# Performance work log

Measured on AMD Instinct MI355X. Metric: run time of the kernel, lower is better.

## Reference

```python
import jax, jax.numpy as jnp
import numpy as np

NEG_SLOPE = 0.2

def _glorot(key, shape):
    fan_in, fan_out = shape[0], shape[1]
    lim = (6.0 / (fan_in + fan_out)) ** 0.5
    return jax.random.uniform(key, shape, jnp.float32, -lim, lim)

def setup_inputs() -> dict:
    key = jax.random.key(0)
    N, E = 50000, 1000000
    node_dim, edge_dim, hidden = 64, 16, 32
    H1 = 4
    ks = jax.random.split(key, 20)
    x = jax.random.normal(ks[0], (N, node_dim), jnp.float32)
    edge_index = jax.random.randint(ks[1], (2, E), 0, N, jnp.int64)
    edge_attr = jax.random.normal(ks[2], (E, edge_dim), jnp.float32)
    d = dict(x=x, edge_index=edge_index, edge_attr=edge_attr)
    # gat1: GATv2Conv(node_dim -> hidden, heads=4, edge_dim)
    d['W1l'] = _glorot(ks[3], (node_dim, H1 * hidden)); d['b1l'] = jnp.zeros((H1 * hidden,), jnp.float32)
    d['W1r'] = _glorot(ks[4], (node_dim, H1 * hidden)); d['b1r'] = jnp.zeros((H1 * hidden,), jnp.float32)
    d['W1e'] = _glorot(ks[5], (edge_dim, H1 * hidden))
    d['att1'] = _glorot(ks[6], (H1, hidden))
    d['bias1'] = jnp.zeros((H1 * hidden,), jnp.float32)
    # gat2: GATv2Conv(4*hidden -> hidden, heads=1, edge_dim)
    d['W2l'] = _glorot(ks[7], (H1 * hidden, hidden)); d['b2l'] = jnp.zeros((hidden,), jnp.float32)
    d['W2r'] = _glorot(ks[8], (H1 * hidden, hidden)); d['b2r'] = jnp.zeros((hidden,), jnp.float32)
    d['W2e'] = _glorot(ks[9], (edge_dim, hidden))
    d['att2'] = _glorot(ks[10], (1, hidden))
    d['bias2'] = jnp.zeros((hidden,), jnp.float32)
    # edge classifier: Linear(2*hidden+edge_dim -> hidden), ReLU, Linear(hidden -> 1)
    ein = 2 * hidden + edge_dim
    d['Wc1'] = _glorot(ks[11], (ein, hidden)); d['bc1'] = jnp.zeros((hidden,), jnp.float32)
    d['Wc2'] = _glorot(ks[12], (hidden, 1)); d['bc2'] = jnp.zeros((1,), jnp.float32)
    return d

def _gatv2(x, src, dst, eattr, Wl, bl, Wr, br, We, att, bias, H, C):
    # src/dst already include self loops; eattr matches.
    N = x.shape[0]
    xl = (x @ Wl + bl).reshape(N, H, C)   # source transform
    xr = (x @ Wr + br).reshape(N, H, C)   # target transform
    ea = (eattr @ We).reshape(-1, H, C)
    m = jax.nn.leaky_relu(xl[src] + xr[dst] + ea, NEG_SLOPE)   # [E,H,C]
    alpha = jnp.einsum('ehc,hc->eh', m, att)                   # [E,H]
    amax = jax.ops.segment_max(alpha, dst, num_segments=N)
    ealpha = jnp.exp(alpha - amax[dst])
    denom = jax.ops.segment_sum(ealpha, dst, num_segments=N)
    alpha = ealpha / denom[dst]
    out = jax.ops.segment_sum(xl[src] * alpha[..., None], dst, num_segments=N)
    return out.reshape(N, H * C) + bias

def reference(x, edge_index, edge_attr, W1l, b1l, W1r, b1r, W1e, att1, bias1,
              W2l, b2l, W2r, b2r, W2e, att2, bias2, Wc1, bc1, Wc2, bc2):
    N = x.shape[0]
    src, dst = edge_index[0], edge_index[1]
    # add self loops with edge_attr fill_value='mean' (per-target mean of incoming edge attrs)
    loop_attr = jax.ops.segment_sum(edge_attr, dst, num_segments=N)
    deg = jax.ops.segment_sum(jnp.ones((dst.shape[0],), edge_attr.dtype), dst, num_segments=N)
    loop_attr = loop_attr / jnp.maximum(deg, 1.0)[:, None]
    ar = jnp.arange(N, dtype=src.dtype)
    src2 = jnp.concatenate([src, ar]); dst2 = jnp.concatenate([dst, ar])
    eattr2 = jnp.concatenate([edge_attr, loop_attr], axis=0)
    h = _gatv2(x, src2, dst2, eattr2, W1l, b1l, W1r, b1r, W1e, att1, bias1, 4, 32)
    h = jax.nn.elu(h)
    h = _gatv2(h, src2, dst2, eattr2, W2l, b2l, W2r, b2r, W2e, att2, bias2, 1, 32)
    h = jax.nn.elu(h)
    edge_emb = jnp.concatenate([h[src], h[dst]], axis=1)         # [E, 2*hidden]
    feats = jnp.concatenate([edge_emb, edge_attr], axis=1)       # [E, 2*hidden+edge_dim]
    hid = jax.nn.relu(feats @ Wc1 + bc1)
    logits = (hid @ Wc2 + bc2).squeeze(-1)                        # [E]
    return logits
```

## Files before the change

kernel.cpp:

```cpp
#include <hip/hip_runtime.h>

namespace {

constexpr int NN  = 50000;
constexpr int EE  = 1000000;
constexpr int EE2 = EE + NN;
constexpr int ND  = 64;
constexpr int F1  = 128;
constexpr int F2  = 32;
constexpr float NEG = 0.2f;

typedef unsigned short ushort_t;
typedef _Float16 half_t;
typedef _Float16 half2_t __attribute__((ext_vector_type(2)));

__device__ __forceinline__ unsigned short f2h(float f) {
  union { half_t h; unsigned short u; } c; c.h = (half_t)f; return c.u;
}
__device__ __forceinline__ float h2f(unsigned short v) {
  union { unsigned short u; half_t h; } c; c.u = v; return (float)c.h;
}
__device__ __forceinline__ half2_t u2h2(unsigned u) {
  union { unsigned u; half2_t h; } c; c.u = u; return c.h;
}
__device__ __forceinline__ unsigned pack2(float x, float y) {
  return (unsigned)f2h(x) | ((unsigned)f2h(y) << 16);
}
__device__ __forceinline__ half2_t mkh2(float x, float y) {
  half2_t r; r.x = (half_t)x; r.y = (half_t)y; return r;
}

#if __has_builtin(__builtin_amdgcn_fdot2)
#define FDOT2(a, b, c) __builtin_amdgcn_fdot2((a), (b), (c), false)
#else
#define FDOT2(a, b, c) ((float)(a).x * (float)(b).x + (float)(a).y * (float)(b).y + (c))
#endif

__global__ __launch_bounds__(256) void k_deg(const int* __restrict__ ei,
                                             int* __restrict__ deg) {
  int e = blockIdx.x * 256 + threadIdx.x;
  if (e < EE) atomicAdd(&deg[ei[EE + e]], 1);
}

__global__ __launch_bounds__(1024) void k_scan(const int* __restrict__ deg,
                                               int* __restrict__ rowstart) {
  __shared__ int sh[1024];
  int t = threadIdx.x;
  int base = t * 49;
  int end = base + 49; if (end > NN) end = NN;
  int s = 0;
  for (int i = base; i < end; ++i) s += deg[i] + 1;
  sh[t] = s;
  __syncthreads();
  for (int off = 1; off < 1024; off <<= 1) {
    int v = (t >= off) ? sh[t - off] : 0;
    __syncthreads();
    sh[t] += v;
    __syncthreads();
  }
  int run = (t == 0) ? 0 : sh[t - 1];
  for (int i = base; i < end; ++i) { rowstart[i] = run; run += deg[i] + 1; }
  if (t == 1023) rowstart[NN] = sh[1023];
}

__global__ __launch_bounds__(256) void k_fill(const int* __restrict__ ei,
                                              const float* __restrict__ edge_attr,
                                              const int* __restrict__ rowstart,
                                              int* __restrict__ cursor,
                                              int2* __restrict__ esd,
                                              ushort_t* __restrict__ eperm,
                                              int* __restrict__ loopos) {
  int i = blockIdx.x * 256 + threadIdx.x;
  if (i >= EE2) return;
  int sn, d;
  if (i < EE) { sn = ei[i]; d = ei[EE + i]; }
  else        { sn = i - EE; d = sn; }
  int pos = rowstart[d] + atomicAdd(&cursor[d], 1);
  esd[pos] = make_int2(sn, d);
  if (i < EE) {
    const float4* s4 = (const float4*)(edge_attr + (size_t)i * 16);
    float4 a = s4[0], b = s4[1], c = s4[2], e = s4[3];
    uint4 lo, hi;
    lo.x = pack2(a.x, a.y); lo.y = pack2(a.z, a.w);
    lo.z = pack2(b.x, b.y); lo.w = pack2(b.z, b.w);
    hi.x = pack2(c.x, c.y); hi.y = pack2(c.z, c.w);
    hi.z = pack2(e.x, e.y); hi.w = pack2(e.z, e.w);
    uint4* t4 = (uint4*)(eperm + (size_t)pos * 16);
    t4[0] = lo; t4[1] = hi;
  } else {
    loopos[d] = pos;
  }
}

__global__ __launch_bounds__(256) void k_loopattr(const int* __restrict__ rowstart,
                                                  const int* __restrict__ loopos,
                                                  ushort_t* __restrict__ eperm) {
  int tid = blockIdx.x * 256 + threadIdx.x;
  if (tid >= NN * 16) return;
  int n = tid >> 4, k = tid & 15;
  int s = rowstart[n], t = rowstart[n + 1];
  int lp = loopos[n];
  float acc = 0.f;
  for (int i = s; i < t; ++i) {
    if (i != lp) acc += h2f(eperm[(size_t)i * 16 + k]);
  }
  float dg = (float)(t - s - 1);
  eperm[(size_t)lp * 16 + k] = f2h(acc / fmaxf(dg, 1.f));
}

__global__ __launch_bounds__(256) void k_xprep(const float* __restrict__ x,
                                               unsigned* __restrict__ xh) {
  int tid = blockIdx.x * 256 + threadIdx.x;
  if (tid >= NN * 32) return;
  float2 v = ((const float2*)x)[tid];
  xh[tid] = pack2(v.x, v.y);
}

__global__ __launch_bounds__(256) void k_wprep(const float* __restrict__ W1l,
                                               const float* __restrict__ W1r,
                                               const float* __restrict__ W2l,
                                               const float* __restrict__ W2r,
                                               unsigned* __restrict__ W1lp,
                                               unsigned* __restrict__ W1rp,
                                               unsigned* __restrict__ W2lp,
                                               unsigned* __restrict__ W2rp) {
  int tid = blockIdx.x * 256 + threadIdx.x;
  if (tid < 32 * 128) {
    int kp = tid >> 7, j = tid & 127;
    W1lp[tid] = pack2(W1l[(2 * kp) * F1 + j], W1l[(2 * kp + 1) * F1 + j]);
    W1rp[tid] = pack2(W1r[(2 * kp) * F1 + j], W1r[(2 * kp + 1) * F1 + j]);
  }
  if (tid < 64 * 32) {
    int kp = tid >> 5, c = tid & 31;
    W2lp[tid] = pack2(W2l[(2 * kp) * F2 + c], W2l[(2 * kp + 1) * F2 + c]);
    W2rp[tid] = pack2(W2r[(2 * kp) * F2 + c], W2r[(2 * kp + 1) * F2 + c]);
  }
}

__global__ __launch_bounds__(256) void k_xform1(const unsigned* __restrict__ xh,
                                                const unsigned* __restrict__ W1lp,
                                                const unsigned* __restrict__ W1rp,
                                                const float* __restrict__ b1l,
                                                const float* __restrict__ b1r,
                                                ushort_t* __restrict__ xlh,
                                                ushort_t* __restrict__ xrh) {
  int tid = blockIdx.x * 256 + threadIdx.x;
  if (tid >= NN * 32) return;
  int n = tid >> 5, g = tid & 31;
  float4 bl = *(const float4*)(b1l + 4 * g);
  float4 br = *(const float4*)(b1r + 4 * g);
  float al0 = bl.x, al1 = bl.y, al2 = bl.z, al3 = bl.w;
  float ar0 = br.x, ar1 = br.y, ar2 = br.z, ar3 = br.w;
  const uint4* xp = (const uint4*)(xh + (size_t)n * 32);
  const uint4* wl = (const uint4*)W1lp;
  const uint4* wr = (const uint4*)W1rp;
#pragma unroll
  for (int kq = 0; kq < 8; ++kq) {
    uint4 xq = xp[kq];
    unsigned xs[4] = {xq.x, xq.y, xq.z, xq.w};
#pragma unroll
    for (int i = 0; i < 4; ++i) {
      int kp = 4 * kq + i;
      uint4 a = wl[kp * 32 + g];
      uint4 b = wr[kp * 32 + g];
      half2_t xv = u2h2(xs[i]);
      al0 = FDOT2(xv, u2h2(a.x), al0);
      al1 = FDOT2(xv, u2h2(a.y), al1);
      al2 = FDOT2(xv, u2h2(a.z), al2);
      al3 = FDOT2(xv, u2h2(a.w), al3);
      ar0 = FDOT2(xv, u2h2(b.x), ar0);
      ar1 = FDOT2(xv, u2h2(b.y), ar1);
      ar2 = FDOT2(xv, u2h2(b.z), ar2);
      ar3 = FDOT2(xv, u2h2(b.w), ar3);
    }
  }
  uint2 ol, orr;
  ol.x = pack2(al0, al1); ol.y = pack2(al2, al3);
  orr.x = pack2(ar0, ar1); orr.y = pack2(ar2, ar3);
  *(uint2*)(xlh + (size_t)n * F1 + 4 * g) = ol;
  *(uint2*)(xrh + (size_t)n * F1 + 4 * g) = orr;
}

__global__ __launch_bounds__(256, 4) void k_alpha1(const ushort_t* __restrict__ eperm,
                                                   const int2* __restrict__ esd,
                                                   const ushort_t* __restrict__ xlh,
                                                   const ushort_t* __restrict__ xrh,
                                                   const float* __restrict__ W1e,
                                                   const float* __restrict__ att1,
                                                   float* __restrict__ alpha1) {
  int lane = threadIdx.x & 63;
  int h = lane >> 4, q = lane & 15, j = h * 32 + 2 * q;
  half2_t w0p[8], w1p[8];
#pragma unroll
  for (int k = 0; k < 8; ++k) {
    w0p[k] = mkh2(W1e[(2 * k) * F1 + j],     W1e[(2 * k + 1) * F1 + j]);
    w1p[k] = mkh2(W1e[(2 * k) * F1 + j + 1], W1e[(2 * k + 1) * F1 + j + 1]);
  }
  float a0 = att1[j], a1 = att1[j + 1];
  int wid = (blockIdx.x * 256 + threadIdx.x) >> 6;
  int nw  = (gridDim.x * 256) >> 6;
  if (wid >= EE2) return;
  const int last = EE2 - 1;

  int2 sd1 = esd[min(wid + nw, last)];
  int2 sd0 = esd[wid];
  const uint4* ep0 = (const uint4*)(eperm + (size_t)wid * 16);
  uint4 ca = ep0[0], cb = ep0[1];
  unsigned ul = *(const unsigned*)(xlh + (size_t)sd0.x * F1 + j);
  unsigned ur = *(const unsigned*)(xrh + (size_t)sd0.y * F1 + j);

  for (int pos = wid; pos <= last; pos += nw) {
    int2 sd2 = esd[min(pos + 2 * nw, last)];
    const uint4* epn = (const uint4*)(eperm + (size_t)min(pos + nw, last) * 16);
    uint4 na = epn[0], nb = epn[1];
    unsigned uln = *(const unsigned*)(xlh + (size_t)sd1.x * F1 + j);
    unsigned urn = *(const unsigned*)(xrh + (size_t)sd1.y * F1 + j);
    half2_t e2[8];
    e2[0] = u2h2(ca.x); e2[1] = u2h2(ca.y); e2[2] = u2h2(ca.z); e2[3] = u2h2(ca.w);
    e2[4] = u2h2(cb.x); e2[5] = u2h2(cb.y); e2[6] = u2h2(cb.z); e2[7] = u2h2(cb.w);
    float ea0 = 0.f, ea1 = 0.f;
#pragma unroll
    for (int k = 0; k < 8; ++k) {
      ea0 = FDOT2(e2[k], w0p[k], ea0);
      ea1 = FDOT2(e2[k], w1p[k], ea1);
    }
    half2_t ul2 = u2h2(ul), ur2 = u2h2(ur);
    float m0 = (float)ul2.x + (float)ur2.x + ea0;
    float m1 = (float)ul2.y + (float)ur2.y + ea1;
    m0 = fmaxf(m0, NEG * m0);
    m1 = fmaxf(m1, NEG * m1);
    float p = a0 * m0 + a1 * m1;
#pragma unroll
    for (int m = 8; m >= 1; m >>= 1) p += __shfl_xor(p, m);
    if (q == 0) alpha1[(size_t)pos * 4 + h] = p;
    sd1 = sd2; ca = na; cb = nb; ul = uln; ur = urn;
  }
}

__global__ __launch_bounds__(256) void k_gatB1(const int2* __restrict__ esd,
                                               const int* __restrict__ rowstart,
                                               const float* __restrict__ alpha1,
                                               const ushort_t* __restrict__ xlh,
                                               const float* __restrict__ bias1,
                                               unsigned* __restrict__ h1h) {
  int n = (blockIdx.x * 256 + threadIdx.x) >> 6;
  if (n >= NN) return;
  int lane = threadIdx.x & 63;
  int h = lane >> 4;
  int s = rowstart[n], t = rowstart[n + 1];
  const int* srcp = (const int*)esd;
  float d = 0.f, acc0 = 0.f, acc1 = 0.f;
  for (int i = s; i < t; i += 4) {
    int i1 = min(i + 1, t - 1), i2 = min(i + 2, t - 1), i3 = min(i + 3, t - 1);
    int s0 = srcp[2 * i], s1 = srcp[2 * i1], s2 = srcp[2 * i2], s3 = srcp[2 * i3];
    float A0 = alpha1[(size_t)i * 4 + h];
    float A1 = alpha1[(size_t)i1 * 4 + h];
    float A2 = alpha1[(size_t)i2 * 4 + h];
    float A3 = alpha1[(size_t)i3 * 4 + h];
    unsigned g0 = *(const unsigned*)(xlh + (size_t)s0 * F1 + 2 * lane);
    unsigned g1 = *(const unsigned*)(xlh + (size_t)s1 * F1 + 2 * lane);
    unsigned g2 = *(const unsigned*)(xlh + (size_t)s2 * F1 + 2 * lane);
    unsigned g3 = *(const unsigned*)(xlh + (size_t)s3 * F1 + 2 * lane);
    float W0 = __expf(A0);
    float W1 = (i + 1 < t) ? __expf(A1) : 0.f;
    float W2 = (i + 2 < t) ? __expf(A2) : 0.f;
    float W3 = (i + 3 < t) ? __expf(A3) : 0.f;
    d += W0 + W1 + W2 + W3;
    half2_t h0 = u2h2(g0), h1v = u2h2(g1), h2v = u2h2(g2), h3v = u2h2(g3);
    acc0 += (float)h0.x * W0 + (float)h1v.x * W1 + (float)h2v.x * W2 + (float)h3v.x * W3;
    acc1 += (float)h0.y * W0 + (float)h1v.y * W1 + (float)h2v.y * W2 + (float)h3v.y * W3;
  }
  float2 bs = *(const float2*)(bias1 + 2 * lane);
  float o0 = acc0 / d + bs.x;
  float o1 = acc1 / d + bs.y;
  o0 = o0 > 0.f ? o0 : (__expf(o0) - 1.f);
  o1 = o1 > 0.f ? o1 : (__expf(o1) - 1.f);
  h1h[(size_t)n * 64 + lane] = pack2(o0, o1);
}

__global__ __launch_bounds__(256) void k_xform2(const unsigned* __restrict__ h1h,
                                                const unsigned* __restrict__ W2lp,
                                                const unsigned* __restrict__ W2rp,
                                                const float* __restrict__ b2l,
                                                const float* __restrict__ b2r,
                                                ushort_t* __restrict__ xl2h,
                                                ushort_t* __restrict__ xr2h) {
  int tid = blockIdx.x * 256 + threadIdx.x;
  if (tid >= NN * 8) return;
  int n = tid >> 3, g = tid & 7;
  float4 bl = *(const float4*)(b2l + 4 * g);
  float4 br = *(const float4*)(b2r + 4 * g);
  float al0 = bl.x, al1 = bl.y, al2 = bl.z, al3 = bl.w;
  float ar0 = br.x, ar1 = br.y, ar2 = br.z, ar3 = br.w;
  const uint4* hp = (const uint4*)(h1h + (size_t)n * 64);
  const uint4* wl = (const uint4*)W2lp;
  const uint4* wr = (const uint4*)W2rp;
#pragma unroll 4
  for (int kq = 0; kq < 16; ++kq) {
    uint4 hq = hp[kq];
    unsigned hs[4] = {hq.x, hq.y, hq.z, hq.w};
#pragma unroll
    for (int i = 0; i < 4; ++i) {
      int kp = 4 * kq + i;
      uint4 a = wl[kp * 8 + g];
      uint4 b = wr[kp * 8 + g];
      half2_t hv = u2h2(hs[i]);
      al0 = FDOT2(hv, u2h2(a.x), al0);
      al1 = FDOT2(hv, u2h2(a.y), al1);
      al2 = FDOT2(hv, u2h2(a.z), al2);
      al3 = FDOT2(hv, u2h2(a.w), al3);
      ar0 = FDOT2(hv, u2h2(b.x), ar0);
      ar1 = FDOT2(hv, u2h2(b.y), ar1);
      ar2 = FDOT2(hv, u2h2(b.z), ar2);
      ar3 = FDOT2(hv, u2h2(b.w), ar3);
    }
  }
  uint2 ol, orr;
  ol.x = pack2(al0, al1); ol.y = pack2(al2, al3);
  orr.x = pack2(ar0, ar1); orr.y = pack2(ar2, ar3);
  *(uint2*)(xl2h + (size_t)n * F2 + 4 * g) = ol;
  *(uint2*)(xr2h + (size_t)n * F2 + 4 * g) = orr;
}

__global__ __launch_bounds__(256, 4) void k_alpha2(const ushort_t* __restrict__ eperm,
                                                   const int2* __restrict__ esd,
                                                   const ushort_t* __restrict__ xl2h,
                                                   const ushort_t* __restrict__ xr2h,
                                                   const float* __restrict__ W2e,
                                                   const float* __restrict__ att2,
                                                   float* __restrict__ alpha2) {
  int lane = threadIdx.x & 63;
  int g = lane >> 4, q = lane & 15, j = 2 * q;
  half2_t w0p[8], w1p[8];
#pragma unroll
  for (int k = 0; k < 8; ++k) {
    w0p[k] = mkh2(W2e[(2 * k) * F2 + j],     W2e[(2 * k + 1) * F2 + j]);
    w1p[k] = mkh2(W2e[(2 * k) * F2 + j + 1], W2e[(2 * k + 1) * F2 + j + 1]);
  }
  float a0 = att2[j], a1 = att2[j + 1];
  int wid = (blockIdx.x * 256 + threadIdx.x) >> 6;
  int nw  = (gridDim.x * 256) >> 6;
  const int st = nw * 4;
  const int last = EE2 - 1;
  int base0 = wid * 4;
  if (base0 >= EE2) return;

  int2 sd1 = esd[min(base0 + st + g, last)];
  int2 sd0 = esd[min(base0 + g, last)];
  const uint4* ep0 = (const uint4*)(eperm + (size_t)min(base0 + g, last) * 16);
  uint4 ca = ep0[0], cb = ep0[1];
  unsigned ul = *(const unsigned*)(xl2h + (size_t)sd0.x * F2 + j);
  unsigned ur = *(const unsigned*)(xr2h + (size_t)sd0.y * F2 + j);

  for (int base = base0; base < EE2; base += st) {
    int2 sd2 = esd[min(base + 2 * st + g, last)];
    const uint4* epn = (const uint4*)(eperm + (size_t)min(base + st + g, last) * 16);
    uint4 na = epn[0], nb = epn[1];
    unsigned uln = *(const unsigned*)(xl2h + (size_t)sd1.x * F2 + j);
    unsigned urn = *(const unsigned*)(xr2h + (size_t)sd1.y * F2 + j);
    half2_t e2[8];
    e2[0] = u2h2(ca.x); e2[1] = u2h2(ca.y); e2[2] = u2h2(ca.z); e2[3] = u2h2(ca.w);
    e2[4] = u2h2(cb.x); e2[5] = u2h2(cb.y); e2[6] = u2h2(cb.z); e2[7] = u2h2(cb.w);
    float ea = 0.f, eb = 0.f;
#pragma unroll
    for (int k = 0; k < 8; ++k) {
      ea = FDOT2(e2[k], w0p[k], ea);
      eb = FDOT2(e2[k], w1p[k], eb);
    }
    half2_t ul2 = u2h2(ul), ur2 = u2h2(ur);
    float m0 = (float)ul2.x + (float)ur2.x + ea;
    float m1 = (float)ul2.y + (float)ur2.y + eb;
    m0 = fmaxf(m0, NEG * m0);
    m1 = fmaxf(m1, NEG * m1);
    float p = a0 * m0 + a1 * m1;
#pragma unroll
    for (int m = 8; m >= 1; m >>= 1) p += __shfl_xor(p, m);
    int pos = base + g;
    if (q == 0 && pos < EE2) alpha2[pos] = p;
    sd1 = sd2; ca = na; cb = nb; ul = uln; ur = urn;
  }
}

__global__ __launch_bounds__(256) void k_gatB2(const int2* __restrict__ esd,
                                               const int* __restrict__ rowstart,
                                               const float* __restrict__ alpha2,
                                               const ushort_t* __restrict__ xl2h,
                                               const float* __restrict__ bias2,
                                               float* __restrict__ h2) {
  int n = (blockIdx.x * 256 + threadIdx.x) >> 4;
  if (n >= NN) return;
  int q = threadIdx.x & 15;
  int s = rowstart[n], t = rowstart[n + 1];
  const int* srcp = (const int*)esd;
  float d = 0.f, acc0 = 0.f, acc1 = 0.f;
  for (int i = s; i < t; i += 4) {
    int i1 = min(i + 1, t - 1), i2 = min(i + 2, t - 1), i3 = min(i + 3, t - 1);
    int s0 = srcp[2 * i], s1 = srcp[2 * i1], s2 = srcp[2 * i2], s3 = srcp[2 * i3];
    float A0 = alpha2[i], A1 = alpha2[i1], A2 = alpha2[i2], A3 = alpha2[i3];
    unsigned g0 = *(const unsigned*)(xl2h + (size_t)s0 * F2 + 2 * q);
    unsigned g1 = *(const unsigned*)(xl2h + (size_t)s1 * F2 + 2 * q);
    unsigned g2 = *(const unsigned*)(xl2h + (size_t)s2 * F2 + 2 * q);
    unsigned g3 = *(const unsigned*)(xl2h + (size_t)s3 * F2 + 2 * q);
    float W0 = __expf(A0);
    float W1 = (i + 1 < t) ? __expf(A1) : 0.f;
    float W2 = (i + 2 < t) ? __expf(A2) : 0.f;
    float W3 = (i + 3 < t) ? __expf(A3) : 0.f;
    d += W0 + W1 + W2 + W3;
    half2_t h0 = u2h2(g0), h1v = u2h2(g1), h2v = u2h2(g2), h3v = u2h2(g3);
    acc0 += (float)h0.x * W0 + (float)h1v.x * W1 + (float)h2v.x * W2 + (float)h3v.x * W3;
    acc1 += (float)h0.y * W0 + (float)h1v.y * W1 + (float)h2v.y * W2 + (float)h3v.y * W3;
  }
  float2 bs = *(const float2*)(bias2 + 2 * q);
  float o0 = acc0 / d + bs.x;
  float o1 = acc1 / d + bs.y;
  o0 = o0 > 0.f ? o0 : (__expf(o0) - 1.f);
  o1 = o1 > 0.f ? o1 : (__expf(o1) - 1.f);
  *(float2*)(h2 + (size_t)n * F2 + 2 * q) = make_float2(o0, o1);
}

__global__ __launch_bounds__(256) void k_ucls(const float* __restrict__ h2,
                                              const float* __restrict__ Wc1,
                                              float* __restrict__ us,
                                              float* __restrict__ ud) {
  int tid = blockIdx.x * 256 + threadIdx.x;
  if (tid >= NN * F2) return;
  int n = tid >> 5, c = tid & 31;
  const float* hp = h2 + (size_t)n * F2;
  float a = 0.f, b = 0.f;
#pragma unroll 8
  for (int k = 0; k < 32; ++k) {
    float hv = hp[k];
    a += hv * Wc1[k * F2 + c];
    b += hv * Wc1[(32 + k) * F2 + c];
  }
  us[tid] = a;
  ud[tid] = b;
}

__global__ __launch_bounds__(256, 4) void k_cls(const int* __restrict__ ei,
                                                const float* __restrict__ edge_attr,
                                                const float* __restrict__ us,
                                                const float* __restrict__ ud,
                                                const float* __restrict__ Wc1,
                                                const float* __restrict__ bc1,
                                                const float* __restrict__ Wc2,
                                                const float* __restrict__ bc2,
                                                float* __restrict__ out) {
  int lane = threadIdx.x & 63;
  int g = lane >> 4, q = lane & 15, j = 2 * q;
  float wk0[16], wk1[16];
#pragma unroll
  for (int k = 0; k < 16; ++k) {
    wk0[k] = Wc1[(64 + k) * F2 + j];
    wk1[k] = Wc1[(64 + k) * F2 + j + 1];
  }
  float b0 = bc1[j], b1 = bc1[j + 1], c0 = Wc2[j], c1 = Wc2[j + 1];
  float bb = bc2[0];
  int wid = (blockIdx.x * 256 + threadIdx.x) >> 6;
  int nw  = (gridDim.x * 256) >> 6;
  const int st = nw * 4;
  const int last = EE - 1;
  int base0 = wid * 4;
  if (base0 >= EE) return;

  int e1c = min(base0 + st + g, last);
  int sn1 = ei[e1c], dn1 = ei[EE + e1c];
  int e0c = min(base0 + g, last);
  int sn0 = ei[e0c], dn0 = ei[EE + e0c];
  const float4* ep0 = (const float4*)(edge_attr + (size_t)e0c * 16);
  float4 ca0 = ep0[0], ca1 = ep0[1], ca2 = ep0[2], ca3 = ep0[3];
  float2 su = *(const float2*)(us + (size_t)sn0 * F2 + j);
  float2 du = *(const float2*)(ud + (size_t)dn0 * F2 + j);

  for (int base = base0; base < EE; base += st) {
    int e2c = min(base + 2 * st + g, last);
    int sn2 = ei[e2c], dn2 = ei[EE + e2c];
    const float4* epn = (const float4*)(edge_attr + (size_t)min(base + st + g, last) * 16);
    float4 na0 = epn[0], na1 = epn[1], na2 = epn[2], na3 = epn[3];
    float2 sun = *(const float2*)(us + (size_t)sn1 * F2 + j);
    float2 dun = *(const float2*)(ud + (size_t)dn1 * F2 + j);
    float ev[16] = {ca0.x, ca0.y, ca0.z, ca0.w, ca1.x, ca1.y, ca1.z, ca1.w,
                    ca2.x, ca2.y, ca2.z, ca2.w, ca3.x, ca3.y, ca3.z, ca3.w};
    float acc0 = b0 + su.x + du.x;
    float acc1 = b1 + su.y + du.y;
#pragma unroll
    for (int k = 0; k < 16; ++k) { acc0 += ev[k] * wk0[k]; acc1 += ev[k] * wk1[k]; }
    float r = fmaxf(acc0, 0.f) * c0 + fmaxf(acc1, 0.f) * c1;
#pragma unroll
    for (int m = 8; m >= 1; m >>= 1) r += __shfl_xor(r, m);
    int e = base + g;
    if (q == 0 && e < EE) out[e] = r + bb;
    sn1 = sn2; dn1 = dn2;
    ca0 = na0; ca1 = na1; ca2 = na2; ca3 = na3;
    su = sun; du = dun;
  }
}

}

extern "C" void kernel_launch(void* const* d_in, const int* in_sizes, int n_in,
                              void* d_out, int out_size, void* d_ws, size_t ws_size,
                              hipStream_t stream) {
  const float* x         = (const float*)d_in[0];
  const int*   ei        = (const int*)d_in[1];
  const float* edge_attr = (const float*)d_in[2];
  const float* W1l  = (const float*)d_in[3];
  const float* b1l  = (const float*)d_in[4];
  const float* W1r  = (const float*)d_in[5];
  const float* b1r  = (const float*)d_in[6];
  const float* W1e  = (const float*)d_in[7];
  const float* att1 = (const float*)d_in[8];
  const float* bias1= (const float*)d_in[9];
  const float* W2l  = (const float*)d_in[10];
  const float* b2l  = (const float*)d_in[11];
  const float* W2r  = (const float*)d_in[12];
  const float* b2r  = (const float*)d_in[13];
  const float* W2e  = (const float*)d_in[14];
  const float* att2 = (const float*)d_in[15];
  const float* bias2= (const float*)d_in[16];
  const float* Wc1  = (const float*)d_in[17];
  const float* bc1  = (const float*)d_in[18];
  const float* Wc2  = (const float*)d_in[19];
  const float* bc2  = (const float*)d_in[20];
  float* out = (float*)d_out;

  int*  deg      = (int*)d_ws;
  int*  cursor   = deg + NN;
  int*  loopos   = cursor + NN;
  int*  rowstart = loopos + NN;
  int2* esd      = (int2*)(rowstart + 50004 + 4);
  ushort_t* eperm = (ushort_t*)(esd + EE2);
  ushort_t* xlh  = eperm + (size_t)EE2 * 16;
  ushort_t* xrh  = xlh + (size_t)NN * F1;
  float* alpha1  = (float*)(xrh + (size_t)NN * F1);
  unsigned* h1h  = (unsigned*)(alpha1 + (size_t)EE2 * 4);
  unsigned* xh   = h1h + (size_t)NN * 64;
  unsigned* W1lp = xh + (size_t)NN * 32;
  unsigned* W1rp = W1lp + 4096;
  unsigned* W2lp = W1rp + 4096;
  unsigned* W2rp = W2lp + 2048;
  ushort_t* xl2h = xlh;
  ushort_t* xr2h = xl2h + (size_t)NN * F2;
  float* alpha2 = (float*)(xr2h + (size_t)NN * F2);
  float* h2 = alpha2 + EE2;
  float* us = h2 + (size_t)NN * F2;
  float* ud = us + (size_t)NN * F2;

  hipMemsetAsync(deg, 0, 2 * (size_t)NN * sizeof(int), stream);

  k_deg<<<(EE + 255) / 256, 256, 0, stream>>>(ei, deg);
  k_scan<<<1, 1024, 0, stream>>>(deg, rowstart);
  k_fill<<<(EE2 + 255) / 256, 256, 0, stream>>>(ei, edge_attr, rowstart, cursor,
                                                esd, eperm, loopos);
  k_loopattr<<<(NN * 16 + 255) / 256, 256, 0, stream>>>(rowstart, loopos, eperm);
  k_xprep<<<(NN * 32 + 255) / 256, 256, 0, stream>>>(x, xh);
  k_wprep<<<16, 256, 0, stream>>>(W1l, W1r, W2l, W2r, W1lp, W1rp, W2lp, W2rp);
  k_xform1<<<(NN * 32 + 255) / 256, 256, 0, stream>>>(xh, W1lp, W1rp, b1l, b1r, xlh, xrh);
  k_alpha1<<<2048, 256, 0, stream>>>(eperm, esd, xlh, xrh, W1e, att1, alpha1);
  k_gatB1<<<(NN * 64 + 255) / 256, 256, 0, stream>>>(esd, rowstart, alpha1, xlh, bias1, h1h);
  k_xform2<<<(NN * 8 + 255) / 256, 256, 0, stream>>>(h1h, W2lp, W2rp, b2l, b2r, xl2h, xr2h);
  k_alpha2<<<2048, 256, 0, stream>>>(eperm, esd, xl2h, xr2h, W2e, att2, alpha2);
  k_gatB2<<<(NN * 16 + 255) / 256, 256, 0, stream>>>(esd, rowstart, alpha2, xl2h, bias2, h2);
  k_ucls<<<(NN * F2 + 255) / 256, 256, 0, stream>>>(h2, Wc1, us, ud);
  k_cls<<<2048, 256, 0, stream>>>(ei, edge_attr, us, ud, Wc1, bc1, Wc2, bc2, out);
}
```

Before: 641.5 us.

## Give each wave contiguous edge chunks, reuse dst rows, move exp into alpha kernels

The alpha1, alpha2 and edge-classifier kernels now hand each wave one contiguous chunk of edges instead of a grid-stride interleave. This improves locality in the dst-sorted edge arrays. In alpha1 the xr row load is skipped when consecutive edges share a destination, which is common because edges are dst-sorted. The exp of the attention logit moves from the gather kernels into the alpha kernels, so each edge is exponentiated once instead of once per gathering lane. The risk is load imbalance from the chunked schedule and a less even memory access spread across waves.

```diff
diff --git a/kernel.cpp b/kernel.cpp
--- a/kernel.cpp
+++ b/kernel.cpp
@@ -197,24 +197,30 @@
     w1p[k] = mkh2(W1e[(2 * k) * F1 + j + 1], W1e[(2 * k + 1) * F1 + j + 1]);
   }
   float a0 = att1[j], a1 = att1[j + 1];
-  int wid = (blockIdx.x * 256 + threadIdx.x) >> 6;
   int nw  = (gridDim.x * 256) >> 6;
-  if (wid >= EE2) return;
+  int wid = __builtin_amdgcn_readfirstlane((blockIdx.x * 256 + threadIdx.x) >> 6);
+  int C = (EE2 + nw - 1) / nw;
+  int start = wid * C;
+  if (start >= EE2) return;
+  int end = min(start + C, EE2);
   const int last = EE2 - 1;
 
-  int2 sd1 = esd[min(wid + nw, last)];
-  int2 sd0 = esd[wid];
-  const uint4* ep0 = (const uint4*)(eperm + (size_t)wid * 16);
+  int2 sd0 = esd[start];
+  int2 sd1 = esd[min(start + 1, last)];
+  const uint4* ep0 = (const uint4*)(eperm + (size_t)start * 16);
   uint4 ca = ep0[0], cb = ep0[1];
   unsigned ul = *(const unsigned*)(xlh + (size_t)sd0.x * F1 + j);
   unsigned ur = *(const unsigned*)(xrh + (size_t)sd0.y * F1 + j);
-
-  for (int pos = wid; pos <= last; pos += nw) {
-    int2 sd2 = esd[min(pos + 2 * nw, last)];
-    const uint4* epn = (const uint4*)(eperm + (size_t)min(pos + nw, last) * 16);
+  int dsty = sd0.y;
+
+  for (int pos = start; pos < end; ++pos) {
+    int np1 = min(pos + 1, last);
+    int2 sd2 = esd[min(pos + 2, last)];
+    const uint4* epn = (const uint4*)(eperm + (size_t)np1 * 16);
     uint4 na = epn[0], nb = epn[1];
     unsigned uln = *(const unsigned*)(xlh + (size_t)sd1.x * F1 + j);
-    unsigned urn = *(const unsigned*)(xrh + (size_t)sd1.y * F1 + j);
+    unsigned urn = (sd1.y != dsty) ? *(const unsigned*)(xrh + (size_t)sd1.y * F1 + j)
+                                   : ur;
     half2_t e2[8];
     e2[0] = u2h2(ca.x); e2[1] = u2h2(ca.y); e2[2] = u2h2(ca.z); e2[3] = u2h2(ca.w);
     e2[4] = u2h2(cb.x); e2[5] = u2h2(cb.y); e2[6] = u2h2(cb.z); e2[7] = u2h2(cb.w);
@@ -232,7 +238,9 @@
     float p = a0 * m0 + a1 * m1;
 #pragma unroll
     for (int m = 8; m >= 1; m >>= 1) p += __shfl_xor(p, m);
-    if (q == 0) alpha1[(size_t)pos * 4 + h] = p;
+    float pe = __expf(p);
+    if (q == 0) alpha1[(size_t)pos * 4 + h] = pe;
+    dsty = sd1.y;
     sd1 = sd2; ca = na; cb = nb; ul = uln; ur = urn;
   }
 }
@@ -253,18 +261,14 @@
   for (int i = s; i < t; i += 4) {
     int i1 = min(i + 1, t - 1), i2 = min(i + 2, t - 1), i3 = min(i + 3, t - 1);
     int s0 = srcp[2 * i], s1 = srcp[2 * i1], s2 = srcp[2 * i2], s3 = srcp[2 * i3];
-    float A0 = alpha1[(size_t)i * 4 + h];
-    float A1 = alpha1[(size_t)i1 * 4 + h];
-    float A2 = alpha1[(size_t)i2 * 4 + h];
-    float A3 = alpha1[(size_t)i3 * 4 + h];
+    float W0 = alpha1[(size_t)i * 4 + h];
+    float W1 = (i + 1 < t) ? alpha1[(size_t)i1 * 4 + h] : 0.f;
+    float W2 = (i + 2 < t) ? alpha1[(size_t)i2 * 4 + h] : 0.f;
+    float W3 = (i + 3 < t) ? alpha1[(size_t)i3 * 4 + h] : 0.f;
     unsigned g0 = *(const unsigned*)(xlh + (size_t)s0 * F1 + 2 * lane);
     unsigned g1 = *(const unsigned*)(xlh + (size_t)s1 * F1 + 2 * lane);
     unsigned g2 = *(const unsigned*)(xlh + (size_t)s2 * F1 + 2 * lane);
     unsigned g3 = *(const unsigned*)(xlh + (size_t)s3 * F1 + 2 * lane);
-    float W0 = __expf(A0);
-    float W1 = (i + 1 < t) ? __expf(A1) : 0.f;
-    float W2 = (i + 2 < t) ? __expf(A2) : 0.f;
-    float W3 = (i + 3 < t) ? __expf(A3) : 0.f;
     d += W0 + W1 + W2 + W3;
     half2_t h0 = u2h2(g0), h1v = u2h2(g1), h2v = u2h2(g2), h3v = u2h2(g3);
     acc0 += (float)h0.x * W0 + (float)h1v.x * W1 + (float)h2v.x * W2 + (float)h3v.x * W3;
@@ -338,23 +342,25 @@
     w1p[k] = mkh2(W2e[(2 * k) * F2 + j + 1], W2e[(2 * k + 1) * F2 + j + 1]);
   }
   float a0 = att2[j], a1 = att2[j + 1];
-  int wid = (blockIdx.x * 256 + threadIdx.x) >> 6;
   int nw  = (gridDim.x * 256) >> 6;
-  const int st = nw * 4;
+  int wid = __builtin_amdgcn_readfirstlane((blockIdx.x * 256 + threadIdx.x) >> 6);
+  int C = (((EE2 + nw - 1) / nw) + 3) & ~3;
+  int start = wid * C;
+  if (start >= EE2) return;
+  int end = min(start + C, EE2);
   const int last = EE2 - 1;
-  int base0 = wid * 4;
-  if (base0 >= EE2) return;
-
-  int2 sd1 = esd[min(base0 + st + g, last)];
-  int2 sd0 = esd[min(base0 + g, last)];
-  const uint4* ep0 = (const uint4*)(eperm + (size_t)min(base0 + g, last) * 16);
+
+  int p0 = min(start + g, last);
+  int2 sd0 = esd[p0];
+  int2 sd1 = esd[min(start + 4 + g, last)];
+  const uint4* ep0 = (const uint4*)(eperm + (size_t)p0 * 16);
   uint4 ca = ep0[0], cb = ep0[1];
   unsigned ul = *(const unsigned*)(xl2h + (size_t)sd0.x * F2 + j);
   unsigned ur = *(const unsigned*)(xr2h + (size_t)sd0.y * F2 + j);
 
-  for (int base = base0; base < EE2; base += st) {
-    int2 sd2 = esd[min(base + 2 * st + g, last)];
-    const uint4* epn = (const uint4*)(eperm + (size_t)min(base + st + g, last) * 16);
+  for (int base = start; base < end; base += 4) {
+    int2 sd2 = esd[min(base + 8 + g, last)];
+    const uint4* epn = (const uint4*)(eperm + (size_t)min(base + 4 + g, last) * 16);
     uint4 na = epn[0], nb = epn[1];
     unsigned uln = *(const unsigned*)(xl2h + (size_t)sd1.x * F2 + j);
     unsigned urn = *(const unsigned*)(xr2h + (size_t)sd1.y * F2 + j);
@@ -375,8 +381,9 @@
     float p = a0 * m0 + a1 * m1;
 #pragma unroll
     for (int m = 8; m >= 1; m >>= 1) p += __shfl_xor(p, m);
+    float pe = __expf(p);
     int pos = base + g;
-    if (q == 0 && pos < EE2) alpha2[pos] = p;
+    if (q == 0 && pos < end) alpha2[pos] = pe;
     sd1 = sd2; ca = na; cb = nb; ul = uln; ur = urn;
   }
 }
@@ -396,15 +403,14 @@
   for (int i = s; i < t; i += 4) {
     int i1 = min(i + 1, t - 1), i2 = min(i + 2, t - 1), i3 = min(i + 3, t - 1);
     int s0 = srcp[2 * i], s1 = srcp[2 * i1], s2 = srcp[2 * i2], s3 = srcp[2 * i3];
-    float A0 = alpha2[i], A1 = alpha2[i1], A2 = alpha2[i2], A3 = alpha2[i3];
+    float W0 = alpha2[i];
+    float W1 = (i + 1 < t) ? alpha2[i1] : 0.f;
+    float W2 = (i + 2 < t) ? alpha2[i2] : 0.f;
+    float W3 = (i + 3 < t) ? alpha2[i3] : 0.f;
     unsigned g0 = *(const unsigned*)(xl2h + (size_t)s0 * F2 + 2 * q);
     unsigned g1 = *(const unsigned*)(xl2h + (size_t)s1 * F2 + 2 * q);
     unsigned g2 = *(const unsigned*)(xl2h + (size_t)s2 * F2 + 2 * q);
     unsigned g3 = *(const unsigned*)(xl2h + (size_t)s3 * F2 + 2 * q);
-    float W0 = __expf(A0);
-    float W1 = (i + 1 < t) ? __expf(A1) : 0.f;
-    float W2 = (i + 2 < t) ? __expf(A2) : 0.f;
-    float W3 = (i + 3 < t) ? __expf(A3) : 0.f;
     d += W0 + W1 + W2 + W3;
     half2_t h0 = u2h2(g0), h1v = u2h2(g1), h2v = u2h2(g2), h3v = u2h2(g3);
     acc0 += (float)h0.x * W0 + (float)h1v.x * W1 + (float)h2v.x * W2 + (float)h3v.x * W3;
@@ -456,26 +462,27 @@
   }
   float b0 = bc1[j], b1 = bc1[j + 1], c0 = Wc2[j], c1 = Wc2[j + 1];
   float bb = bc2[0];
-  int wid = (blockIdx.x * 256 + threadIdx.x) >> 6;
   int nw  = (gridDim.x * 256) >> 6;
-  const int st = nw * 4;
+  int wid = __builtin_amdgcn_readfirstlane((blockIdx.x * 256 + threadIdx.x) >> 6);
+  int C = (((EE + nw - 1) / nw) + 3) & ~3;
+  int start = wid * C;
+  if (start >= EE) return;
+  int end = min(start + C, EE);
   const int last = EE - 1;
-  int base0 = wid * 4;
-  if (base0 >= EE) return;
-
-  int e1c = min(base0 + st + g, last);
+
+  int e0c = min(start + g, last);
+  int sn0 = ei[e0c], dn0 = ei[EE + e0c];
+  int e1c = min(start + 4 + g, last);
   int sn1 = ei[e1c], dn1 = ei[EE + e1c];
-  int e0c = min(base0 + g, last);
-  int sn0 = ei[e0c], dn0 = ei[EE + e0c];
   const float4* ep0 = (const float4*)(edge_attr + (size_t)e0c * 16);
   float4 ca0 = ep0[0], ca1 = ep0[1], ca2 = ep0[2], ca3 = ep0[3];
   float2 su = *(const float2*)(us + (size_t)sn0 * F2 + j);
   float2 du = *(const float2*)(ud + (size_t)dn0 * F2 + j);
 
-  for (int base = base0; base < EE; base += st) {
-    int e2c = min(base + 2 * st + g, last);
+  for (int base = start; base < end; base += 4) {
+    int e2c = min(base + 8 + g, last);
     int sn2 = ei[e2c], dn2 = ei[EE + e2c];
-    const float4* epn = (const float4*)(edge_attr + (size_t)min(base + st + g, last) * 16);
+    const float4* epn = (const float4*)(edge_attr + (size_t)min(base + 4 + g, last) * 16);
     float4 na0 = epn[0], na1 = epn[1], na2 = epn[2], na3 = epn[3];
     float2 sun = *(const float2*)(us + (size_t)sn1 * F2 + j);
     float2 dun = *(const float2*)(ud + (size_t)dn1 * F2 + j);
@@ -489,7 +496,7 @@
 #pragma unroll
     for (int m = 8; m >= 1; m >>= 1) r += __shfl_xor(r, m);
     int e = base + g;
-    if (q == 0 && e < EE) out[e] = r + bb;
+    if (q == 0 && e < end) out[e] = r + bb;
     sn1 = sn2; dn1 = dn2;
     ca0 = na0; ca1 = na1; ca2 = na2; ca3 = na3;
     su = sun; du = dun;
```

New measurement: 602.7 us. 6.0% less time.
